# Kernel tuning notes

Hardware: AMD Instinct MI355X
Metric: run time of the kernel (lower is better)

Reference implementation:

```python
import jax, jax.numpy as jnp
import numpy as np

N = 100000
E = 1600000
D_IN, D_HID, D_OUT = 128, 128, 128


def gcn_conv(x, edge_index, W, b):
    """PyG GCNConv with default symmetric normalization and added self-loops.
    out = D^{-1/2} (A + I) D^{-1/2} (x W) + b, edge weights = 1.
    """
    n = x.shape[0]
    h = x @ W                                   # [N, D_out]
    src, dst = edge_index[0], edge_index[1]     # messages flow src -> dst
    ones = jnp.ones(src.shape[0], dtype=x.dtype)
    # degree includes the self-loop (+1), computed on the target index as in PyG
    deg = jax.ops.segment_sum(ones, dst, num_segments=n) + 1.0  # [N]
    dinv = jax.lax.rsqrt(deg)                   # deg >= 1 so safe
    norm = dinv[src] * dinv[dst]                # [E]
    msg = h[src] * norm[:, None]                # [E, D_out]
    agg = jax.ops.segment_sum(msg, dst, num_segments=n)
    # self-loop contribution: norm = dinv_i * dinv_i = 1/deg_i
    out = agg + h * (dinv * dinv)[:, None] + b
    return out


def layer_norm(x, gamma, beta, eps=1e-5):
    mu = jnp.mean(x, axis=-1, keepdims=True)
    var = jnp.mean(jnp.square(x - mu), axis=-1, keepdims=True)
    return (x - mu) * jax.lax.rsqrt(var + eps) * gamma + beta


def setup_inputs() -> dict:
    key = jax.random.key(0)
    ks = jax.random.split(key, 8)
    x = jax.random.normal(ks[0], (N, D_IN), dtype=jnp.float32)
    edge_index = jax.random.randint(ks[1], (2, E), 0, N, dtype=jnp.int64)
    s1 = 1.0 / np.sqrt(D_IN)
    s2 = 1.0 / np.sqrt(D_HID)
    W1 = jax.random.uniform(ks[2], (D_IN, D_HID), jnp.float32, -s1, s1)
    b1 = jnp.zeros((D_HID,), jnp.float32)
    W2 = jax.random.uniform(ks[3], (D_HID, D_OUT), jnp.float32, -s2, s2)
    b2 = jnp.zeros((D_OUT,), jnp.float32)
    gamma = jnp.ones((D_OUT,), jnp.float32)
    beta = jnp.zeros((D_OUT,), jnp.float32)
    return {"x": x, "edge_index": edge_index, "W1": W1, "b1": b1,
            "W2": W2, "b2": b2, "gamma": gamma, "beta": beta}


def reference(x, edge_index, W1, b1, W2, b2, gamma, beta):
    h = gcn_conv(x, edge_index, W1, b1)
    h = jax.nn.relu(h)
    # dropout is identity in eval mode (deterministic reference)
    h = gcn_conv(h, edge_index, W2, b2)
    return layer_norm(h, gamma, beta)
```

## Files before the change

kernel.cpp:

```cpp
#include <hip/hip_runtime.h>


#define N_NODES 100000
#define N_EDGES 1600000
#define NBLK_N  391
#define NB      196
#define BKT_CAP 8960
#define BIN_GRID 391
#define GEMM_GRID 1563

typedef unsigned int  u32;
typedef unsigned short u16;
typedef unsigned char u8;
typedef __attribute__((ext_vector_type(8))) short bf16x8;
typedef __attribute__((ext_vector_type(4))) float f32x4;

__device__ __forceinline__ float bflo(u32 u){ return __uint_as_float(u << 16); }
__device__ __forceinline__ float bfhi(u32 u){ return __uint_as_float(u & 0xFFFF0000u); }
__device__ __forceinline__ u32 f2b(float f){
  u32 u = __float_as_uint(f);
  return (u + 0x7FFFu + ((u >> 16) & 1u)) >> 16;
}
__device__ __forceinline__ u32 pack2(float a, float b){ return f2b(a) | (f2b(b) << 16); }
__device__ __forceinline__ u32 clampN(int s){
  u32 u = (u32)s;
  return (u < (u32)N_NODES) ? u : (u32)(N_NODES - 1);
}

__global__ __launch_bounds__(256) void detect_init(const int* __restrict__ ei,
                                                   int* __restrict__ flags,
                                                   u32* __restrict__ bucket_fill){
  int t = threadIdx.x;
  if (t < NB) bucket_fill[t] = 0;
  if (t < 64){
    int nzodd = (ei[2 * t + 1] != 0) ? 1 : 0;
    #pragma unroll
    for (int o = 32; o > 0; o >>= 1) nzodd += __shfl_xor(nzodd, o, 64);
    if (t == 0) flags[1] = (nzodd == 0) ? 1 : 0;
  }
}


__device__ __forceinline__ void build_wfrag(u16* wfrag, const float* __restrict__ W,
                                            int tid){
  #pragma unroll
  for (int i = 0; i < 8; ++i){
    int fid   = tid + i * 256;
    int lane  = fid & 63;
    int kb    = (fid >> 6) & 3;
    int ntile = fid >> 8;
    int n  = ntile * 16 + (lane & 15);
    int k0 = kb * 32 + (lane >> 4) * 8;
    u16 tmp[8];
    #pragma unroll
    for (int j = 0; j < 8; ++j) tmp[j] = (u16)f2b(W[(k0 + j) * 128 + n]);
    *(bf16x8*)(wfrag + (size_t)fid * 8) = *(const bf16x8*)tmp;
  }
}

__device__ __forceinline__ void gemm_tail(const u16* wfrag, const bf16x8 afrag[4],
                                          int rowbase, int lane,
                                          u16* __restrict__ Hout, int nrows){
  const int m = lane & 15, q = lane >> 4;
  f32x4 acc[8];
  #pragma unroll
  for (int n = 0; n < 8; ++n) acc[n] = (f32x4){0.f, 0.f, 0.f, 0.f};
  #pragma unroll
  for (int n = 0; n < 8; ++n){
    #pragma unroll
    for (int kb = 0; kb < 4; ++kb){
      bf16x8 bfrag = *(const bf16x8*)(wfrag + ((size_t)(n * 4 + kb) * 64 + lane) * 8);
      acc[n] = __builtin_amdgcn_mfma_f32_16x16x32_bf16(afrag[kb], bfrag, acc[n], 0, 0, 0);
    }
  }
  #pragma unroll
  for (int r = 0; r < 4; ++r){
    int orow = rowbase + q * 4 + r;
    if (orow < nrows){
      u16* Or = Hout + (size_t)orow * 128 + m;
      #pragma unroll
      for (int n = 0; n < 8; ++n) Or[n * 16] = (u16)f2b(acc[n][r]);
    }
  }
}

__device__ __forceinline__ void gemm_f32_body(u16* wfrag, const float* __restrict__ A,
                                              const float* __restrict__ W,
                                              u16* __restrict__ Hout, int nrows, int bid){
  build_wfrag(wfrag, W, threadIdx.x);
  __syncthreads();
  const int lane = threadIdx.x & 63;
  const int wv   = threadIdx.x >> 6;
  const int rowbase = bid * 64 + wv * 16;
  const int row  = rowbase + (lane & 15);
  const int rowc = (row < nrows) ? row : (nrows - 1);
  const int q    = lane >> 4;
  bf16x8 afrag[4];
  const float* Ar = A + (size_t)rowc * 128;
  #pragma unroll
  for (int kb = 0; kb < 4; ++kb){
    f32x4 p0 = *(const f32x4*)(Ar + kb * 32 + q * 8);
    f32x4 p1 = *(const f32x4*)(Ar + kb * 32 + q * 8 + 4);
    bf16x8 f;
    f[0] = (short)f2b(p0[0]); f[1] = (short)f2b(p0[1]);
    f[2] = (short)f2b(p0[2]); f[3] = (short)f2b(p0[3]);
    f[4] = (short)f2b(p1[0]); f[5] = (short)f2b(p1[1]);
    f[6] = (short)f2b(p1[2]); f[7] = (short)f2b(p1[3]);
    afrag[kb] = f;
  }
  gemm_tail(wfrag, afrag, rowbase, lane, Hout, nrows);
}

__device__ __forceinline__ void gemm_bf16_body(u16* wfrag, const u16* __restrict__ A,
                                               const float* __restrict__ W,
                                               u16* __restrict__ Hout, int nrows, int bid){
  build_wfrag(wfrag, W, threadIdx.x);
  __syncthreads();
  const int lane = threadIdx.x & 63;
  const int wv   = threadIdx.x >> 6;
  const int rowbase = bid * 64 + wv * 16;
  const int row  = rowbase + (lane & 15);
  const int rowc = (row < nrows) ? row : (nrows - 1);
  const int q    = lane >> 4;
  bf16x8 afrag[4];
  const u16* Ar = A + (size_t)rowc * 128;
  #pragma unroll
  for (int kb = 0; kb < 4; ++kb)
    afrag[kb] = *(const bf16x8*)(Ar + kb * 32 + q * 8);
  gemm_tail(wfrag, afrag, rowbase, lane, Hout, nrows);
}


__device__ __forceinline__ void binA_body(u32* cnt ,
                                          const int* __restrict__ ei,
                                          const int* __restrict__ flags,
                                          u32* __restrict__ binned,
                                          u32* __restrict__ bucket_fill, int bb){
  u32* gbase = cnt + 256;
  const int tid = threadIdx.x;
  cnt[tid] = 0;
  __syncthreads();
  const int i64  = flags[1];
  const int base = bb * 4096;
  u32 pk[16], rk[16], bk[16];
  #pragma unroll
  for (int j = 0; j < 16; ++j){
    int e = base + tid + j * 256;
    bk[j] = 0xFFFFFFFFu;
    if (e < N_EDGES){
      int dsti = i64 ? ei[2 * N_EDGES + 2 * e] : ei[N_EDGES + e];
      int srci = i64 ? ei[2 * e]               : ei[e];
      u32 ud = clampN(dsti), us = clampN(srci);
      u32 b = ud >> 9;
      bk[j] = b;
      pk[j] = us | ((ud & 511u) << 17);
      rk[j] = atomicAdd(&cnt[b], 1u);
    }
  }
  __syncthreads();
  u32 c = cnt[tid];
  u32 old = 0;
  if (c) old = atomicAdd(&bucket_fill[tid < NB ? tid : 0], tid < NB ? c : 0u);
  gbase[tid] = old;
  __syncthreads();
  #pragma unroll
  for (int j = 0; j < 16; ++j){
    if (bk[j] != 0xFFFFFFFFu){
      u32 idx = gbase[bk[j]] + rk[j];
      if (idx < BKT_CAP) binned[(size_t)bk[j] * BKT_CAP + idx] = pk[j];
    }
  }
}


__global__ __launch_bounds__(256) void fused_gemm_bin(const float* __restrict__ A,
                                                      const float* __restrict__ W,
                                                      u16* __restrict__ Hout,
                                                      const int* __restrict__ ei,
                                                      const int* __restrict__ flags,
                                                      u32* __restrict__ binned,
                                                      u32* __restrict__ bucket_fill){
  __shared__ u16 smem[16384];
  if (blockIdx.x < GEMM_GRID){
    gemm_f32_body(smem, A, W, Hout, N_NODES, blockIdx.x);
  } else {
    binA_body((u32*)smem, ei, flags, binned, bucket_fill, blockIdx.x - GEMM_GRID);
  }
}

__global__ __launch_bounds__(256) void gemm_f32in(const float* __restrict__ A,
                                                  const float* __restrict__ W,
                                                  u16* __restrict__ Hout){
  __shared__ u16 smem[16384];
  gemm_f32_body(smem, A, W, Hout, N_NODES, blockIdx.x);
}
__global__ __launch_bounds__(256) void gemm_bf16in(const u16* __restrict__ A,
                                                   const float* __restrict__ W,
                                                   u16* __restrict__ Hout){
  __shared__ u16 smem[16384];
  gemm_bf16_body(smem, A, W, Hout, N_NODES, blockIdx.x);
}


__global__ __launch_bounds__(256) void fill_sort(const u32* __restrict__ binned,
                                                 const u32* __restrict__ bucket_fill,
                                                 int* __restrict__ offs,
                                                 float* __restrict__ dinv,
                                                 int* __restrict__ srclist){
  __shared__ u32 cnt[512];
  __shared__ u32 sc[512];
  __shared__ u32 red[256];
  const int b   = blockIdx.x;
  const int tid = threadIdx.x;
  cnt[tid] = 0; cnt[tid + 256] = 0;
  __syncthreads();

  u32 n = bucket_fill[b]; if (n > BKT_CAP) n = BKT_CAP;
  const u32* eb = binned + (size_t)b * BKT_CAP;

  for (u32 i = tid; i < n; i += 256)
    atomicAdd(&cnt[eb[i] >> 17], 1u);

  u32 v = 0;
  if (tid < b && tid < NB){
    u32 f = bucket_fill[tid];
    v = (f > BKT_CAP) ? BKT_CAP : f;
  }
  red[tid] = v;
  __syncthreads();
  for (int o = 128; o > 0; o >>= 1){
    if (tid < o) red[tid] += red[tid + o];
    __syncthreads();
  }
  const u32 base = red[0];
  __syncthreads();

  u32 pair = cnt[2 * tid] + cnt[2 * tid + 1];
  red[tid] = pair;
  __syncthreads();
  for (int o = 1; o < 256; o <<= 1){
    u32 add = (tid >= o) ? red[tid - o] : 0;
    __syncthreads();
    red[tid] += add;
    __syncthreads();
  }
  u32 pex = red[tid] - pair;
  sc[2 * tid]     = pex;
  sc[2 * tid + 1] = pex + cnt[2 * tid];
  __syncthreads();

  const u32 basenode = (u32)b << 9;
  #pragma unroll
  for (int h = 0; h < 2; ++h){
    u32 l = tid + h * 256;
    u32 node = basenode + l;
    if (node < (u32)N_NODES){
      offs[node] = (int)(base + sc[l]);
      dinv[node] = rsqrtf((float)cnt[l] + 1.0f);
    }
  }
  if (b == NB - 1 && tid == 0) offs[N_NODES] = (int)(base + n);

  __syncthreads();
  cnt[tid] = 0; cnt[tid + 256] = 0;
  __syncthreads();
  for (u32 i = tid; i < n; i += 256){
    u32 pk = eb[i];
    u32 d  = pk >> 17;
    u32 r  = atomicAdd(&cnt[d], 1u);
    srclist[base + sc[d] + r] = (int)(pk & 0x1FFFFu);
  }
}


__global__ __launch_bounds__(256) void count_deg(const int* __restrict__ ei,
                                                 const int* __restrict__ flags,
                                                 int* __restrict__ deg){
  int e   = blockIdx.x * 256 + threadIdx.x;
  int i64 = flags[1];
  int dst = i64 ? ei[2 * N_EDGES + 2 * e] : ei[N_EDGES + e];
  if ((unsigned)dst < (unsigned)N_NODES) atomicAdd(&deg[dst], 1);
}

__global__ __launch_bounds__(256) void fill_edges(const int* __restrict__ ei,
                                                  const int* __restrict__ flags,
                                                  int* __restrict__ woff,
                                                  int* __restrict__ srclist){
  int e   = blockIdx.x * 256 + threadIdx.x;
  int i64 = flags[1];
  int dst = i64 ? ei[2 * N_EDGES + 2 * e] : ei[N_EDGES + e];
  int src = i64 ? ei[2 * e]               : ei[e];
  if ((unsigned)dst < (unsigned)N_NODES){
    int p = atomicAdd(&woff[dst], 1);
    if ((unsigned)p < (unsigned)N_EDGES) srclist[p] = src;
  }
}

__global__ __launch_bounds__(256) void scan1(const int* __restrict__ deg,
                                             int* __restrict__ offs,
                                             int* __restrict__ bsum,
                                             float* __restrict__ dinv){
  __shared__ int sh[256];
  int t = threadIdx.x;
  int i = blockIdx.x * 256 + t;
  int v = (i < N_NODES) ? deg[i] : 0;
  if (i < N_NODES) dinv[i] = rsqrtf((float)v + 1.0f);
  sh[t] = v;
  __syncthreads();
  for (int o = 1; o < 256; o <<= 1){
    int add = (t >= o) ? sh[t - o] : 0;
    __syncthreads();
    sh[t] += add;
    __syncthreads();
  }
  if (i < N_NODES) offs[i] = sh[t] - v;
  if (t == 255)    bsum[blockIdx.x] = sh[255];
}

__global__ __launch_bounds__(512) void scan2(const int* __restrict__ bsum,
                                             int* __restrict__ bofs){
  __shared__ int sh[512];
  int t = threadIdx.x;
  int v = (t < NBLK_N) ? bsum[t] : 0;
  sh[t] = v;
  __syncthreads();
  for (int o = 1; o < 512; o <<= 1){
    int add = (t >= o) ? sh[t - o] : 0;
    __syncthreads();
    sh[t] += add;
    __syncthreads();
  }
  if (t < NBLK_N) bofs[t] = sh[t] - v;
}

__global__ __launch_bounds__(256) void finalize_offs(int* __restrict__ offs,
                                                     const int* __restrict__ bofs,
                                                     int* __restrict__ woff){
  int i = blockIdx.x * 256 + threadIdx.x;
  if (i < N_NODES){
    int o = offs[i] + bofs[blockIdx.x];
    offs[i] = o;
    woff[i] = o;
  }
  if (i == 0) offs[N_NODES] = N_EDGES;
}


#define GATHER_EDGE(sv, A0, A1)                         \
  { u32 s_ = clampN(sv);                                \
    float w_ = dinv[s_];                                \
    u32 h_ = H[s_ * 64 + lane];                         \
    A0 = fmaf(w_, bflo(h_), A0);                        \
    A1 = fmaf(w_, bfhi(h_), A1); }

__global__ __launch_bounds__(256) void gather_relu(const int* __restrict__ offs,
                                                   const int* __restrict__ srcl,
                                                   const u32* __restrict__ H,
                                                   const float* __restrict__ dinv,
                                                   const float* __restrict__ bias,
                                                   u32* __restrict__ X2){
  const int node = blockIdx.x * 4 + (threadIdx.x >> 6);
  const int lane = threadIdx.x & 63;
  int beg = offs[node], end = offs[node + 1];
  if (end > N_EDGES) end = N_EDGES;
  if (beg < 0 || beg > end) beg = end;
  float a0 = 0.f, a1 = 0.f, c0 = 0.f, c1 = 0.f;
  int e = beg;
  for (; e + 8 <= end; e += 8){
    int s0=srcl[e],s1=srcl[e+1],s2=srcl[e+2],s3=srcl[e+3];
    int s4=srcl[e+4],s5=srcl[e+5],s6=srcl[e+6],s7=srcl[e+7];
    GATHER_EDGE(s0,a0,a1) GATHER_EDGE(s1,c0,c1)
    GATHER_EDGE(s2,a0,a1) GATHER_EDGE(s3,c0,c1)
    GATHER_EDGE(s4,a0,a1) GATHER_EDGE(s5,c0,c1)
    GATHER_EDGE(s6,a0,a1) GATHER_EDGE(s7,c0,c1)
  }
  for (; e + 4 <= end; e += 4){
    int s0=srcl[e],s1=srcl[e+1],s2=srcl[e+2],s3=srcl[e+3];
    GATHER_EDGE(s0,a0,a1) GATHER_EDGE(s1,c0,c1)
    GATHER_EDGE(s2,a0,a1) GATHER_EDGE(s3,c0,c1)
  }
  for (; e < end; ++e){ int s0=srcl[e]; GATHER_EDGE(s0,a0,a1) }
  a0 += c0;  a1 += c1;
  float di = dinv[node];
  u32 hs = H[(u32)node * 64 + lane];
  float b0 = bias[2 * lane], b1v = bias[2 * lane + 1];
  float v0 = fmaf(a0, di, fmaf(bflo(hs), di * di, b0));
  float v1 = fmaf(a1, di, fmaf(bfhi(hs), di * di, b1v));
  X2[(u32)node * 64 + lane] = pack2(fmaxf(v0, 0.f), fmaxf(v1, 0.f));
}

__global__ __launch_bounds__(256) void gather_ln(const int* __restrict__ offs,
                                                 const int* __restrict__ srcl,
                                                 const u32* __restrict__ H,
                                                 const float* __restrict__ dinv,
                                                 const float* __restrict__ bias,
                                                 const float* __restrict__ gamma,
                                                 const float* __restrict__ beta,
                                                 float* __restrict__ out){
  const int node = blockIdx.x * 4 + (threadIdx.x >> 6);
  const int lane = threadIdx.x & 63;
  int beg = offs[node], end = offs[node + 1];
  if (end > N_EDGES) end = N_EDGES;
  if (beg < 0 || beg > end) beg = end;
  float a0 = 0.f, a1 = 0.f, c0 = 0.f, c1 = 0.f;
  int e = beg;
  for (; e + 8 <= end; e += 8){
    int s0=srcl[e],s1=srcl[e+1],s2=srcl[e+2],s3=srcl[e+3];
    int s4=srcl[e+4],s5=srcl[e+5],s6=srcl[e+6],s7=srcl[e+7];
    GATHER_EDGE(s0,a0,a1) GATHER_EDGE(s1,c0,c1)
    GATHER_EDGE(s2,a0,a1) GATHER_EDGE(s3,c0,c1)
    GATHER_EDGE(s4,a0,a1) GATHER_EDGE(s5,c0,c1)
    GATHER_EDGE(s6,a0,a1) GATHER_EDGE(s7,c0,c1)
  }
  for (; e + 4 <= end; e += 4){
    int s0=srcl[e],s1=srcl[e+1],s2=srcl[e+2],s3=srcl[e+3];
    GATHER_EDGE(s0,a0,a1) GATHER_EDGE(s1,c0,c1)
    GATHER_EDGE(s2,a0,a1) GATHER_EDGE(s3,c0,c1)
  }
  for (; e < end; ++e){ int s0=srcl[e]; GATHER_EDGE(s0,a0,a1) }
  a0 += c0;  a1 += c1;
  float di = dinv[node];
  u32 hs = H[(u32)node * 64 + lane];
  float b0 = bias[2 * lane], b1v = bias[2 * lane + 1];
  float v0 = fmaf(a0, di, fmaf(bflo(hs), di * di, b0));
  float v1 = fmaf(a1, di, fmaf(bfhi(hs), di * di, b1v));

  float s2 = v0 + v1;
  #pragma unroll
  for (int o = 32; o > 0; o >>= 1) s2 += __shfl_xor(s2, o, 64);
  float mu = s2 * 0.0078125f;
  float d0 = v0 - mu, d1 = v1 - mu;
  float qq = d0 * d0 + d1 * d1;
  #pragma unroll
  for (int o = 32; o > 0; o >>= 1) qq += __shfl_xor(qq, o, 64);
  float rr = rsqrtf(qq * 0.0078125f + 1e-5f);

  float g0 = gamma[2 * lane], g1 = gamma[2 * lane + 1];
  float t0 = beta[2 * lane],  t1 = beta[2 * lane + 1];
  *(float2*)(out + (size_t)node * 128 + 2 * lane) =
      make_float2(fmaf(d0 * rr, g0, t0), fmaf(d1 * rr, g1, t1));
}


extern "C" void kernel_launch(void* const* d_in, const int* in_sizes, int n_in,
                              void* d_out, int out_size, void* d_ws, size_t ws_size,
                              hipStream_t stream){
  const float* x  = (const float*)d_in[0];
  const int*   ei = (const int*)d_in[1];
  const float* W1 = (const float*)d_in[2];
  const float* b1 = (const float*)d_in[3];
  const float* W2 = (const float*)d_in[4];
  const float* b2 = (const float*)d_in[5];
  const float* gm = (const float*)d_in[6];
  const float* bt = (const float*)d_in[7];

  char* ws = (char*)d_ws;
  size_t off = 0;
  auto carve = [&](size_t bytes) -> void* {
    void* p = ws + off;
    off = (off + bytes + 255) & ~(size_t)255;
    return p;
  };
  int*   flags       = (int*)  carve(64);
  u32*   bucket_fill = (u32*)  carve(NB * 4);
  int*   offs        = (int*)  carve((size_t)(N_NODES + 1) * 4);
  float* dinv        = (float*)carve((size_t)N_NODES * 4);
  int*   srclist     = (int*)  carve((size_t)N_EDGES * 4);
  int*   deg         = (int*)  carve((size_t)N_NODES * 4);
  int*   bsum        = (int*)  carve(2048);
  int*   bofs        = (int*)  carve(2048);

  size_t bin_bytes = (size_t)NB * BKT_CAP * 4;
  u32* binned = (u32*)carve(bin_bytes);
  bool use_binned = (ws_size >= off);
  if (!use_binned) off = (size_t)((char*)binned - ws);

  size_t h_bytes = (size_t)N_NODES * 128 * 2;
  u32* H1 = (u32*)d_out;
  u32* X2 = (u32*)d_out + 6400000;
  u32* H2 = (ws_size >= off + h_bytes) ? (u32*)carve(h_bytes) : (u32*)d_in[0];

  detect_init<<<1, 256, 0, stream>>>(ei, flags, bucket_fill);

  if (use_binned){
    fused_gemm_bin<<<GEMM_GRID + BIN_GRID, 256, 0, stream>>>(x, W1, (u16*)H1, ei, flags,
                                                             binned, bucket_fill);
    fill_sort     <<<NB, 256, 0, stream>>>(binned, bucket_fill, offs, dinv, srclist);
  } else {
    hipMemsetAsync(deg, 0, (size_t)N_NODES * 4, stream);
    count_deg     <<<N_EDGES / 256, 256, 0, stream>>>(ei, flags, deg);
    scan1         <<<NBLK_N,        256, 0, stream>>>(deg, offs, bsum, dinv);
    scan2         <<<1,             512, 0, stream>>>(bsum, bofs);
    finalize_offs <<<NBLK_N,        256, 0, stream>>>(offs, bofs, deg );
    fill_edges    <<<N_EDGES / 256, 256, 0, stream>>>(ei, flags, deg , srclist);
    gemm_f32in    <<<GEMM_GRID,     256, 0, stream>>>(x, W1, (u16*)H1);
  }

  gather_relu <<<N_NODES / 4, 256, 0, stream>>>(offs, srclist, H1, dinv, b1, X2);
  gemm_bf16in <<<GEMM_GRID,   256, 0, stream>>>((const u16*)X2, W2, (u16*)H2);
  gather_ln   <<<N_NODES / 4, 256, 0, stream>>>(offs, srclist, H2, dinv, b2, gm, bt,
                                                (float*)d_out);
}
```

Baseline: 313.8 us.

## Gather four edges per wave with 16-byte row loads in GCN aggregation

Both gather kernels now split each 64-lane wave into four 16-lane groups. Each group fetches a whole bf16 feature row with 128-bit loads, so one wave processes eight edges per iteration instead of walking edges one by one with 4-byte loads. Partial sums are combined with cross-group shuffles, and the self-loop, bias, ReLU and LayerNorm epilogues are rewritten to use vector loads and stores. Source clamping moves into fill_edges so the inner loop does less index work. The cost is a larger register footprint, extra shuffle reductions, and masked lanes when a node's degree is not a multiple of eight.

```diff
diff --git a/kernel.cpp b/kernel.cpp
--- a/kernel.cpp
+++ b/kernel.cpp
@@ -14,6 +14,7 @@
 typedef unsigned char u8;
 typedef __attribute__((ext_vector_type(8))) short bf16x8;
 typedef __attribute__((ext_vector_type(4))) float f32x4;
+typedef __attribute__((ext_vector_type(4))) u32 u32x4;
 
 __device__ __forceinline__ float bflo(u32 u){ return __uint_as_float(u << 16); }
 __device__ __forceinline__ float bfhi(u32 u){ return __uint_as_float(u & 0xFFFF0000u); }
@@ -292,7 +293,7 @@
   int src = i64 ? ei[2 * e]               : ei[e];
   if ((unsigned)dst < (unsigned)N_NODES){
     int p = atomicAdd(&woff[dst], 1);
-    if ((unsigned)p < (unsigned)N_EDGES) srclist[p] = src;
+    if ((unsigned)p < (unsigned)N_EDGES) srclist[p] = clampN(src);
   }
 }
 
@@ -346,13 +347,6 @@
 }
 
 
-#define GATHER_EDGE(sv, A0, A1)                         \
-  { u32 s_ = clampN(sv);                                \
-    float w_ = dinv[s_];                                \
-    u32 h_ = H[s_ * 64 + lane];                         \
-    A0 = fmaf(w_, bflo(h_), A0);                        \
-    A1 = fmaf(w_, bfhi(h_), A1); }
-
 __global__ __launch_bounds__(256) void gather_relu(const int* __restrict__ offs,
                                                    const int* __restrict__ srcl,
                                                    const u32* __restrict__ H,
@@ -361,32 +355,52 @@
                                                    u32* __restrict__ X2){
   const int node = blockIdx.x * 4 + (threadIdx.x >> 6);
   const int lane = threadIdx.x & 63;
+  const int grp  = lane >> 4;
+  const int cq   = (lane & 15) * 4;
   int beg = offs[node], end = offs[node + 1];
   if (end > N_EDGES) end = N_EDGES;
   if (beg < 0 || beg > end) beg = end;
-  float a0 = 0.f, a1 = 0.f, c0 = 0.f, c1 = 0.f;
-  int e = beg;
-  for (; e + 8 <= end; e += 8){
-    int s0=srcl[e],s1=srcl[e+1],s2=srcl[e+2],s3=srcl[e+3];
-    int s4=srcl[e+4],s5=srcl[e+5],s6=srcl[e+6],s7=srcl[e+7];
-    GATHER_EDGE(s0,a0,a1) GATHER_EDGE(s1,c0,c1)
-    GATHER_EDGE(s2,a0,a1) GATHER_EDGE(s3,c0,c1)
-    GATHER_EDGE(s4,a0,a1) GATHER_EDGE(s5,c0,c1)
-    GATHER_EDGE(s6,a0,a1) GATHER_EDGE(s7,c0,c1)
-  }
-  for (; e + 4 <= end; e += 4){
-    int s0=srcl[e],s1=srcl[e+1],s2=srcl[e+2],s3=srcl[e+3];
-    GATHER_EDGE(s0,a0,a1) GATHER_EDGE(s1,c0,c1)
-    GATHER_EDGE(s2,a0,a1) GATHER_EDGE(s3,c0,c1)
-  }
-  for (; e < end; ++e){ int s0=srcl[e]; GATHER_EDGE(s0,a0,a1) }
-  a0 += c0;  a1 += c1;
+
+  float a[8] = {0,0,0,0,0,0,0,0};
+  float c[8] = {0,0,0,0,0,0,0,0};
+  for (int e = beg; e < end; e += 8){
+    int e0 = e + grp, e1 = e + 4 + grp;
+    int e0c = (e0 < end) ? e0 : (end - 1);
+    int e1c = (e1 < end) ? e1 : (end - 1);
+    u32 s0 = (u32)srcl[e0c], s1 = (u32)srcl[e1c];
+    float w0 = (e0 < end) ? dinv[s0] : 0.f;
+    float w1 = (e1 < end) ? dinv[s1] : 0.f;
+    u32x4 h0 = *(const u32x4*)(H + (size_t)s0 * 64 + cq);
+    u32x4 h1 = *(const u32x4*)(H + (size_t)s1 * 64 + cq);
+    #pragma unroll
+    for (int k = 0; k < 4; ++k){
+      a[2*k]   = fmaf(w0, bflo(h0[k]), a[2*k]);
+      a[2*k+1] = fmaf(w0, bfhi(h0[k]), a[2*k+1]);
+      c[2*k]   = fmaf(w1, bflo(h1[k]), c[2*k]);
+      c[2*k+1] = fmaf(w1, bfhi(h1[k]), c[2*k+1]);
+    }
+  }
+  #pragma unroll
+  for (int k = 0; k < 8; ++k){
+    a[k] += c[k];
+    a[k] += __shfl_xor(a[k], 16, 64);
+    a[k] += __shfl_xor(a[k], 32, 64);
+  }
+
   float di = dinv[node];
-  u32 hs = H[(u32)node * 64 + lane];
-  float b0 = bias[2 * lane], b1v = bias[2 * lane + 1];
-  float v0 = fmaf(a0, di, fmaf(bflo(hs), di * di, b0));
-  float v1 = fmaf(a1, di, fmaf(bfhi(hs), di * di, b1v));
-  X2[(u32)node * 64 + lane] = pack2(fmaxf(v0, 0.f), fmaxf(v1, 0.f));
+  u32x4 hs = *(const u32x4*)(H + (size_t)node * 64 + cq);
+  f32x4 bA = *(const f32x4*)(bias + 2 * cq);
+  f32x4 bB = *(const f32x4*)(bias + 2 * cq + 4);
+  float bb[8] = {bA[0],bA[1],bA[2],bA[3],bB[0],bB[1],bB[2],bB[3]};
+  u32 outp[4];
+  #pragma unroll
+  for (int k = 0; k < 4; ++k){
+    float vl = fmaf(a[2*k],   di, fmaf(bflo(hs[k]), di*di, bb[2*k]));
+    float vh = fmaf(a[2*k+1], di, fmaf(bfhi(hs[k]), di*di, bb[2*k+1]));
+    outp[k] = pack2(fmaxf(vl, 0.f), fmaxf(vh, 0.f));
+  }
+  if (grp == 0)
+    *(u32x4*)(X2 + (size_t)node * 64 + cq) = (u32x4){outp[0],outp[1],outp[2],outp[3]};
 }
 
 __global__ __launch_bounds__(256) void gather_ln(const int* __restrict__ offs,
@@ -399,46 +413,79 @@
                                                  float* __restrict__ out){
   const int node = blockIdx.x * 4 + (threadIdx.x >> 6);
   const int lane = threadIdx.x & 63;
+  const int grp  = lane >> 4;
+  const int cq   = (lane & 15) * 4;
   int beg = offs[node], end = offs[node + 1];
   if (end > N_EDGES) end = N_EDGES;
   if (beg < 0 || beg > end) beg = end;
-  float a0 = 0.f, a1 = 0.f, c0 = 0.f, c1 = 0.f;
-  int e = beg;
-  for (; e + 8 <= end; e += 8){
-    int s0=srcl[e],s1=srcl[e+1],s2=srcl[e+2],s3=srcl[e+3];
-    int s4=srcl[e+4],s5=srcl[e+5],s6=srcl[e+6],s7=srcl[e+7];
-    GATHER_EDGE(s0,a0,a1) GATHER_EDGE(s1,c0,c1)
-    GATHER_EDGE(s2,a0,a1) GATHER_EDGE(s3,c0,c1)
-    GATHER_EDGE(s4,a0,a1) GATHER_EDGE(s5,c0,c1)
-    GATHER_EDGE(s6,a0,a1) GATHER_EDGE(s7,c0,c1)
-  }
-  for (; e + 4 <= end; e += 4){
-    int s0=srcl[e],s1=srcl[e+1],s2=srcl[e+2],s3=srcl[e+3];
-    GATHER_EDGE(s0,a0,a1) GATHER_EDGE(s1,c0,c1)
-    GATHER_EDGE(s2,a0,a1) GATHER_EDGE(s3,c0,c1)
-  }
-  for (; e < end; ++e){ int s0=srcl[e]; GATHER_EDGE(s0,a0,a1) }
-  a0 += c0;  a1 += c1;
+
+  float a[8] = {0,0,0,0,0,0,0,0};
+  float c[8] = {0,0,0,0,0,0,0,0};
+  for (int e = beg; e < end; e += 8){
+    int e0 = e + grp, e1 = e + 4 + grp;
+    int e0c = (e0 < end) ? e0 : (end - 1);
+    int e1c = (e1 < end) ? e1 : (end - 1);
+    u32 s0 = (u32)srcl[e0c], s1 = (u32)srcl[e1c];
+    float w0 = (e0 < end) ? dinv[s0] : 0.f;
+    float w1 = (e1 < end) ? dinv[s1] : 0.f;
+    u32x4 h0 = *(const u32x4*)(H + (size_t)s0 * 64 + cq);
+    u32x4 h1 = *(const u32x4*)(H + (size_t)s1 * 64 + cq);
+    #pragma unroll
+    for (int k = 0; k < 4; ++k){
+      a[2*k]   = fmaf(w0, bflo(h0[k]), a[2*k]);
+      a[2*k+1] = fmaf(w0, bfhi(h0[k]), a[2*k+1]);
+      c[2*k]   = fmaf(w1, bflo(h1[k]), c[2*k]);
+      c[2*k+1] = fmaf(w1, bfhi(h1[k]), c[2*k+1]);
+    }
+  }
+  #pragma unroll
+  for (int k = 0; k < 8; ++k){
+    a[k] += c[k];
+    a[k] += __shfl_xor(a[k], 16, 64);
+    a[k] += __shfl_xor(a[k], 32, 64);
+  }
+
   float di = dinv[node];
-  u32 hs = H[(u32)node * 64 + lane];
-  float b0 = bias[2 * lane], b1v = bias[2 * lane + 1];
-  float v0 = fmaf(a0, di, fmaf(bflo(hs), di * di, b0));
-  float v1 = fmaf(a1, di, fmaf(bfhi(hs), di * di, b1v));
-
-  float s2 = v0 + v1;
+  u32x4 hs = *(const u32x4*)(H + (size_t)node * 64 + cq);
+  f32x4 bA = *(const f32x4*)(bias + 2 * cq);
+  f32x4 bB = *(const f32x4*)(bias + 2 * cq + 4);
+  float bb[8] = {bA[0],bA[1],bA[2],bA[3],bB[0],bB[1],bB[2],bB[3]};
+  float vv[8];
+  #pragma unroll
+  for (int k = 0; k < 4; ++k){
+    vv[2*k]   = fmaf(a[2*k],   di, fmaf(bflo(hs[k]), di*di, bb[2*k]));
+    vv[2*k+1] = fmaf(a[2*k+1], di, fmaf(bfhi(hs[k]), di*di, bb[2*k+1]));
+  }
+
+  float s2 = 0.f;
+  #pragma unroll
+  for (int k = 0; k < 8; ++k) s2 += vv[k];
   #pragma unroll
   for (int o = 32; o > 0; o >>= 1) s2 += __shfl_xor(s2, o, 64);
-  float mu = s2 * 0.0078125f;
-  float d0 = v0 - mu, d1 = v1 - mu;
-  float qq = d0 * d0 + d1 * d1;
+  float mu = s2 * (1.0f / 512.0f);
+  float dd[8];
+  float qq = 0.f;
+  #pragma unroll
+  for (int k = 0; k < 8; ++k){ dd[k] = vv[k] - mu; qq += dd[k] * dd[k]; }
   #pragma unroll
   for (int o = 32; o > 0; o >>= 1) qq += __shfl_xor(qq, o, 64);
-  float rr = rsqrtf(qq * 0.0078125f + 1e-5f);
-
-  float g0 = gamma[2 * lane], g1 = gamma[2 * lane + 1];
-  float t0 = beta[2 * lane],  t1 = beta[2 * lane + 1];
-  *(float2*)(out + (size_t)node * 128 + 2 * lane) =
-      make_float2(fmaf(d0 * rr, g0, t0), fmaf(d1 * rr, g1, t1));
+  float rr = rsqrtf(qq * (1.0f / 512.0f) + 1e-5f);
+
+  f32x4 gA = *(const f32x4*)(gamma + 2 * cq);
+  f32x4 gB = *(const f32x4*)(gamma + 2 * cq + 4);
+  f32x4 tA = *(const f32x4*)(beta + 2 * cq);
+  f32x4 tB = *(const f32x4*)(beta + 2 * cq + 4);
+  float gg[8] = {gA[0],gA[1],gA[2],gA[3],gB[0],gB[1],gB[2],gB[3]};
+  float tt[8] = {tA[0],tA[1],tA[2],tA[3],tB[0],tB[1],tB[2],tB[3]};
+  if (grp < 2){
+    f32x4 o4;
+    #pragma unroll
+    for (int k = 0; k < 4; ++k){
+      int idx = grp * 4 + k;
+      o4[k] = fmaf(dd[idx] * rr, gg[idx], tt[idx]);
+    }
+    *(f32x4*)(out + (size_t)node * 128 + 2 * cq + grp * 4) = o4;
+  }
 }
 
 
```

Result: slower. 333.3 us (+6.2%).
